# Kernel optimization log

Hardware: AMD Instinct MI355X
Metric: run time of the kernel (lower is better)

## Reference

```python
import jax, jax.numpy as jnp
import numpy as np

B, S, K, N = 4, 2048, 4096, 4096
BLK = 32  # Q4_0 block size along the K (input) dimension


def setup_inputs() -> dict:
    key = jax.random.key(0)
    k1, k2, k3, k4 = jax.random.split(key, 4)
    x = jax.random.normal(k1, (B, S, K), dtype=jnp.float32)
    # 4-bit codes stored unpacked as int32 in [0, 16)
    qweight = jax.random.randint(k2, (N, K), 0, 16, dtype=jnp.int32)
    # one positive fp scale per 32-wide block (typical Q4_0 magnitudes)
    scales = jax.random.uniform(k3, (N, K // BLK), dtype=jnp.float32) * 0.1
    bias = jax.random.normal(k4, (N,), dtype=jnp.float32)
    return {"x": x, "qweight": qweight, "scales": scales, "bias": bias}


def dequantize_q4_0(qweight, scales):
    # w[n, k] = scale[n, k//32] * (q[n, k] - 8)
    n, k = qweight.shape
    q = qweight.reshape(n, k // BLK, BLK).astype(scales.dtype)
    w = (q - 8.0) * scales[:, :, None]
    return w.reshape(n, k)


def reference(x, qweight, scales, bias):
    # dequantize once (cached path), then F.linear(x, w, bias)
    w = dequantize_q4_0(qweight, scales)          # [N, K]
    out = jnp.einsum("bsk,nk->bsn", x, w)          # [B, S, N]
    return out + bias
```

## Files before the change

kernel.cpp:

```cpp
#include <hip/hip_runtime.h>
#include <stdint.h>

#define M_DIM 8192
#define N_DIM 4096
#define K_DIM 4096
#define NKB   (K_DIM / 32)

typedef __bf16 bf16x8 __attribute__((ext_vector_type(8)));
typedef float  f32x4  __attribute__((ext_vector_type(4)));

__device__ __forceinline__ uint32_t pack2_bf16(float lo, float hi) {
    union { float f; uint32_t u; } a, b;
    a.f = lo; b.f = hi;
    return __builtin_amdgcn_perm(b.u + 0x8000u, a.u + 0x8000u, 0x07060302u);
}


__global__ void cvt_x_kernel(const float* __restrict__ x,
                             uint32_t* __restrict__ xb, int n8) {
    int i = blockIdx.x * blockDim.x + threadIdx.x;
    if (i >= n8) return;
    const float4* p = (const float4*)x;
    float4 v0 = p[2 * i], v1 = p[2 * i + 1];
    uint4 o;
    o.x = pack2_bf16(v0.x, v0.y);
    o.y = pack2_bf16(v0.z, v0.w);
    o.z = pack2_bf16(v1.x, v1.y);
    o.w = pack2_bf16(v1.z, v1.w);
    ((uint4*)xb)[i] = o;
}

__global__ void dequant_kernel(const int* __restrict__ q,
                               const float* __restrict__ s,
                               uint32_t* __restrict__ wb, int n8) {
    int i = blockIdx.x * blockDim.x + threadIdx.x;
    if (i >= n8) return;
    int base = i << 3;
    int n = base >> 12;
    int k = base & (K_DIM - 1);
    float sc = s[n * NKB + (k >> 5)];
    float m8 = -8.0f * sc;
    const int4* qp = (const int4*)q;
    int4 q0 = qp[2 * i], q1 = qp[2 * i + 1];
    uint4 o;
    o.x = pack2_bf16(fmaf((float)q0.x, sc, m8), fmaf((float)q0.y, sc, m8));
    o.y = pack2_bf16(fmaf((float)q0.z, sc, m8), fmaf((float)q0.w, sc, m8));
    o.z = pack2_bf16(fmaf((float)q1.x, sc, m8), fmaf((float)q1.y, sc, m8));
    o.w = pack2_bf16(fmaf((float)q1.z, sc, m8), fmaf((float)q1.w, sc, m8));
    ((uint4*)wb)[i] = o;
}

__global__ __launch_bounds__(256)
void gemm_bf16_kernel(const __bf16* __restrict__ A,
                      const __bf16* __restrict__ Bw,
                      const float* __restrict__ bias,
                      float* __restrict__ C) {
    __shared__ __align__(16) __bf16 lA[128 * 32];
    __shared__ __align__(16) __bf16 lB[128 * 32];

    const int t    = threadIdx.x;
    const int wave = t >> 6;
    const int lane = t & 63;
    const int bm = blockIdx.y, bn = blockIdx.x;
    const int wm = wave >> 1, wn = wave & 1;

    const int row0 = t >> 2;
    const int c0   = (t & 3) * 8;
    const __bf16* gA0 = A  + (size_t)(bm * 128 + row0) * K_DIM + c0;
    const __bf16* gA1 = A  + (size_t)(bm * 128 + row0 + 64) * K_DIM + c0;
    const __bf16* gB0 = Bw + (size_t)(bn * 128 + row0) * K_DIM + c0;
    const __bf16* gB1 = Bw + (size_t)(bn * 128 + row0 + 64) * K_DIM + c0;
    __bf16* sA0 = lA + t * 8;
    __bf16* sA1 = lA + (256 + t) * 8;
    __bf16* sB0 = lB + t * 8;
    __bf16* sB1 = lB + (256 + t) * 8;

    const int r = lane & 15, quad = lane >> 4;
    const __bf16* fA = lA + (wm * 64 + r) * 32 + quad * 8;
    const __bf16* fB = lB + (wn * 64 + r) * 32 + quad * 8;

    f32x4 acc[4][4] = {};

    for (int kt = 0; kt < NKB; ++kt) {
        __syncthreads();
        __builtin_amdgcn_global_load_lds(
            (const __attribute__((address_space(1))) uint32_t*)gA0,
            (__attribute__((address_space(3))) uint32_t*)sA0, 16, 0, 0);
        __builtin_amdgcn_global_load_lds(
            (const __attribute__((address_space(1))) uint32_t*)gA1,
            (__attribute__((address_space(3))) uint32_t*)sA1, 16, 0, 0);
        __builtin_amdgcn_global_load_lds(
            (const __attribute__((address_space(1))) uint32_t*)gB0,
            (__attribute__((address_space(3))) uint32_t*)sB0, 16, 0, 0);
        __builtin_amdgcn_global_load_lds(
            (const __attribute__((address_space(1))) uint32_t*)gB1,
            (__attribute__((address_space(3))) uint32_t*)sB1, 16, 0, 0);
        gA0 += 32; gA1 += 32; gB0 += 32; gB1 += 32;
        __syncthreads();

        bf16x8 af[4], bfr[4];
#pragma unroll
        for (int i = 0; i < 4; ++i)
            af[i] = *(const bf16x8*)(fA + i * 16 * 32);
#pragma unroll
        for (int j = 0; j < 4; ++j)
            bfr[j] = *(const bf16x8*)(fB + j * 16 * 32);
#pragma unroll
        for (int i = 0; i < 4; ++i)
#pragma unroll
            for (int j = 0; j < 4; ++j)
                acc[i][j] = __builtin_amdgcn_mfma_f32_16x16x32_bf16(
                    af[i], bfr[j], acc[i][j], 0, 0, 0);
    }

    const int m0 = bm * 128 + wm * 64;
    const int n0 = bn * 128 + wn * 64;
#pragma unroll
    for (int j = 0; j < 4; ++j) {
        int col = n0 + j * 16 + r;
        float bv = bias[col];
#pragma unroll
        for (int i = 0; i < 4; ++i) {
            int rbase = m0 + i * 16 + quad * 4;
#pragma unroll
            for (int e = 0; e < 4; ++e)
                C[(size_t)(rbase + e) * N_DIM + col] = acc[i][j][e] + bv;
        }
    }
}

__global__ __launch_bounds__(256)
void fused_gemm_kernel(const float* __restrict__ X,
                       const int* __restrict__ Q,
                       const float* __restrict__ S,
                       const float* __restrict__ bias,
                       float* __restrict__ C) {
    __shared__ __align__(16) __bf16 lA[128 * 32];
    __shared__ __align__(16) __bf16 lB[128 * 32];

    const int t    = threadIdx.x;
    const int wave = t >> 6;
    const int lane = t & 63;
    const int bm = blockIdx.y, bn = blockIdx.x;
    const int wm = wave >> 1, wn = wave & 1;

    const int srow = t >> 1;
    const int sc0  = (t & 1) << 4;
    const float* gX = X + (size_t)(bm * 128 + srow) * K_DIM + sc0;
    const int*   gQ = Q + (size_t)(bn * 128 + srow) * K_DIM + sc0;
    const float* gS = S + (size_t)(bn * 128 + srow) * NKB;
    __bf16* sA = lA + srow * 32 + sc0;
    __bf16* sB = lB + srow * 32 + sc0;

    const int r = lane & 15, quad = lane >> 4;
    const __bf16* fA = lA + (wm * 64 + r) * 32 + quad * 8;
    const __bf16* fB = lB + (wn * 64 + r) * 32 + quad * 8;

    f32x4 acc[4][4] = {};

    float4 x0 = ((const float4*)gX)[0];
    float4 x1 = ((const float4*)gX)[1];
    float4 x2 = ((const float4*)gX)[2];
    float4 x3 = ((const float4*)gX)[3];
    int4 q0 = ((const int4*)gQ)[0];
    int4 q1 = ((const int4*)gQ)[1];
    int4 q2 = ((const int4*)gQ)[2];
    int4 q3 = ((const int4*)gQ)[3];
    float sc = gS[0];

    for (int kt = 0; kt < NKB; ++kt) {
        uint4 pa0, pa1, pb0, pb1;
        pa0.x = pack2_bf16(x0.x, x0.y); pa0.y = pack2_bf16(x0.z, x0.w);
        pa0.z = pack2_bf16(x1.x, x1.y); pa0.w = pack2_bf16(x1.z, x1.w);
        pa1.x = pack2_bf16(x2.x, x2.y); pa1.y = pack2_bf16(x2.z, x2.w);
        pa1.z = pack2_bf16(x3.x, x3.y); pa1.w = pack2_bf16(x3.z, x3.w);
        float m8 = -8.0f * sc;
        pb0.x = pack2_bf16(fmaf((float)q0.x, sc, m8), fmaf((float)q0.y, sc, m8));
        pb0.y = pack2_bf16(fmaf((float)q0.z, sc, m8), fmaf((float)q0.w, sc, m8));
        pb0.z = pack2_bf16(fmaf((float)q1.x, sc, m8), fmaf((float)q1.y, sc, m8));
        pb0.w = pack2_bf16(fmaf((float)q1.z, sc, m8), fmaf((float)q1.w, sc, m8));
        pb1.x = pack2_bf16(fmaf((float)q2.x, sc, m8), fmaf((float)q2.y, sc, m8));
        pb1.y = pack2_bf16(fmaf((float)q2.z, sc, m8), fmaf((float)q2.w, sc, m8));
        pb1.z = pack2_bf16(fmaf((float)q3.x, sc, m8), fmaf((float)q3.y, sc, m8));
        pb1.w = pack2_bf16(fmaf((float)q3.z, sc, m8), fmaf((float)q3.w, sc, m8));

        __syncthreads();
        *(uint4*)sA = pa0; *(uint4*)(sA + 8) = pa1;
        *(uint4*)sB = pb0; *(uint4*)(sB + 8) = pb1;
        __syncthreads();

        if (kt + 1 < NKB) {
            gX += 32; gQ += 32;
            x0 = ((const float4*)gX)[0];
            x1 = ((const float4*)gX)[1];
            x2 = ((const float4*)gX)[2];
            x3 = ((const float4*)gX)[3];
            q0 = ((const int4*)gQ)[0];
            q1 = ((const int4*)gQ)[1];
            q2 = ((const int4*)gQ)[2];
            q3 = ((const int4*)gQ)[3];
            sc = gS[kt + 1];
        }

        bf16x8 af[4], bfr[4];
#pragma unroll
        for (int i = 0; i < 4; ++i)
            af[i] = *(const bf16x8*)(fA + i * 16 * 32);
#pragma unroll
        for (int j = 0; j < 4; ++j)
            bfr[j] = *(const bf16x8*)(fB + j * 16 * 32);
#pragma unroll
        for (int i = 0; i < 4; ++i)
#pragma unroll
            for (int j = 0; j < 4; ++j)
                acc[i][j] = __builtin_amdgcn_mfma_f32_16x16x32_bf16(
                    af[i], bfr[j], acc[i][j], 0, 0, 0);
    }

    const int m0 = bm * 128 + wm * 64;
    const int n0 = bn * 128 + wn * 64;
#pragma unroll
    for (int j = 0; j < 4; ++j) {
        int col = n0 + j * 16 + r;
        float bv = bias[col];
#pragma unroll
        for (int i = 0; i < 4; ++i) {
            int rbase = m0 + i * 16 + quad * 4;
#pragma unroll
            for (int e = 0; e < 4; ++e)
                C[(size_t)(rbase + e) * N_DIM + col] = acc[i][j][e] + bv;
        }
    }
}

extern "C" void kernel_launch(void* const* d_in, const int* in_sizes, int n_in,
                              void* d_out, int out_size, void* d_ws, size_t ws_size,
                              hipStream_t stream) {
    const float* x    = (const float*)d_in[0];
    const int*   qw   = (const int*)d_in[1];
    const float* sc   = (const float*)d_in[2];
    const float* bias = (const float*)d_in[3];
    float* out = (float*)d_out;

    dim3 grid(N_DIM / 128, M_DIM / 128);

    const size_t need = ((size_t)M_DIM * K_DIM + (size_t)N_DIM * K_DIM) * 2;
    if (ws_size >= need && d_ws != nullptr) {
        uint32_t* xb = (uint32_t*)d_ws;
        uint32_t* wb = xb + (size_t)M_DIM * K_DIM / 2;
        int n8x = M_DIM * K_DIM / 8;
        cvt_x_kernel<<<n8x / 256, 256, 0, stream>>>(x, xb, n8x);
        int n8w = N_DIM * K_DIM / 8;
        dequant_kernel<<<n8w / 256, 256, 0, stream>>>(qw, sc, wb, n8w);
        gemm_bf16_kernel<<<grid, 256, 0, stream>>>(
            (const __bf16*)xb, (const __bf16*)wb, bias, out);
    } else {
        fused_gemm_kernel<<<grid, 256, 0, stream>>>(x, qw, sc, bias, out);
    }
}
```

Measured before the change: 571.0 us.

## Double K tile to 64, XOR-swizzle LDS, overlap next loads with MFMA

The GEMM now stages a 64-wide K slice per iteration instead of 32, halving the number of barrier pairs. LDS is laid out with an XOR swizzle on 16-byte column groups to avoid bank conflicts on fragment reads. Fragments are read into registers first, then the next tile's global-to-LDS loads are issued before the MFMA block so memory latency overlaps compute. The cost is more registers for the doubled fragments, plus a reliance on the async load_lds completing correctly across the barrier.

```diff
diff --git a/kernel.cpp b/kernel.cpp
--- a/kernel.cpp
+++ b/kernel.cpp
@@ -5,6 +5,8 @@
 #define N_DIM 4096
 #define K_DIM 4096
 #define NKB   (K_DIM / 32)
+#define BK    64
+#define KSTEPS (K_DIM / BK)
 
 typedef __bf16 bf16x8 __attribute__((ext_vector_type(8)));
 typedef float  f32x4  __attribute__((ext_vector_type(4)));
@@ -55,8 +57,8 @@
                       const __bf16* __restrict__ Bw,
                       const float* __restrict__ bias,
                       float* __restrict__ C) {
-    __shared__ __align__(16) __bf16 lA[128 * 32];
-    __shared__ __align__(16) __bf16 lB[128 * 32];
+    __shared__ __align__(16) __bf16 lA[128 * BK];
+    __shared__ __align__(16) __bf16 lB[128 * BK];
 
     const int t    = threadIdx.x;
     const int wave = t >> 6;
@@ -64,54 +66,64 @@
     const int bm = blockIdx.y, bn = blockIdx.x;
     const int wm = wave >> 1, wn = wave & 1;
 
-    const int row0 = t >> 2;
-    const int c0   = (t & 3) * 8;
-    const __bf16* gA0 = A  + (size_t)(bm * 128 + row0) * K_DIM + c0;
-    const __bf16* gA1 = A  + (size_t)(bm * 128 + row0 + 64) * K_DIM + c0;
-    const __bf16* gB0 = Bw + (size_t)(bn * 128 + row0) * K_DIM + c0;
-    const __bf16* gB1 = Bw + (size_t)(bn * 128 + row0 + 64) * K_DIM + c0;
-    __bf16* sA0 = lA + t * 8;
-    __bf16* sA1 = lA + (256 + t) * 8;
-    __bf16* sB0 = lB + t * 8;
-    __bf16* sB1 = lB + (256 + t) * 8;
+    const int trow = t >> 3;
+    const int cg   = (t & 7) ^ (trow & 7);
+    const __bf16* gA = A  + (size_t)(bm * 128 + trow) * K_DIM + cg * 8;
+    const __bf16* gB = Bw + (size_t)(bn * 128 + trow) * K_DIM + cg * 8;
+
+#define ISSUE_LOADS()                                                         \
+    do {                                                                      \
+        _Pragma("unroll")                                                     \
+        for (int kk = 0; kk < 4; ++kk) {                                      \
+            __builtin_amdgcn_global_load_lds(                                 \
+                (const __attribute__((address_space(1))) uint32_t*)           \
+                    (gA + (size_t)(32 * kk) * K_DIM),                         \
+                (__attribute__((address_space(3))) uint32_t*)                 \
+                    (lA + (t + 256 * kk) * 8), 16, 0, 0);                     \
+            __builtin_amdgcn_global_load_lds(                                 \
+                (const __attribute__((address_space(1))) uint32_t*)           \
+                    (gB + (size_t)(32 * kk) * K_DIM),                         \
+                (__attribute__((address_space(3))) uint32_t*)                 \
+                    (lB + (t + 256 * kk) * 8), 16, 0, 0);                     \
+        }                                                                     \
+    } while (0)
 
     const int r = lane & 15, quad = lane >> 4;
-    const __bf16* fA = lA + (wm * 64 + r) * 32 + quad * 8;
-    const __bf16* fB = lB + (wn * 64 + r) * 32 + quad * 8;
+    const int s0 = quad ^ (r & 7);
+    const __bf16* fA = lA + (wm * 64 + r) * BK;
+    const __bf16* fB = lB + (wn * 64 + r) * BK;
 
     f32x4 acc[4][4] = {};
 
-    for (int kt = 0; kt < NKB; ++kt) {
-        __syncthreads();
-        __builtin_amdgcn_global_load_lds(
-            (const __attribute__((address_space(1))) uint32_t*)gA0,
-            (__attribute__((address_space(3))) uint32_t*)sA0, 16, 0, 0);
-        __builtin_amdgcn_global_load_lds(
-            (const __attribute__((address_space(1))) uint32_t*)gA1,
-            (__attribute__((address_space(3))) uint32_t*)sA1, 16, 0, 0);
-        __builtin_amdgcn_global_load_lds(
-            (const __attribute__((address_space(1))) uint32_t*)gB0,
-            (__attribute__((address_space(3))) uint32_t*)sB0, 16, 0, 0);
-        __builtin_amdgcn_global_load_lds(
-            (const __attribute__((address_space(1))) uint32_t*)gB1,
-            (__attribute__((address_space(3))) uint32_t*)sB1, 16, 0, 0);
-        gA0 += 32; gA1 += 32; gB0 += 32; gB1 += 32;
-        __syncthreads();
-
-        bf16x8 af[4], bfr[4];
-#pragma unroll
-        for (int i = 0; i < 4; ++i)
-            af[i] = *(const bf16x8*)(fA + i * 16 * 32);
-#pragma unroll
-        for (int j = 0; j < 4; ++j)
-            bfr[j] = *(const bf16x8*)(fB + j * 16 * 32);
-#pragma unroll
-        for (int i = 0; i < 4; ++i)
-#pragma unroll
-            for (int j = 0; j < 4; ++j)
-                acc[i][j] = __builtin_amdgcn_mfma_f32_16x16x32_bf16(
-                    af[i], bfr[j], acc[i][j], 0, 0, 0);
-    }
+    ISSUE_LOADS();
+
+    for (int kt = 0; kt < KSTEPS; ++kt) {
+        __syncthreads();
+        bf16x8 af[2][4], bfr[2][4];
+#pragma unroll
+        for (int i = 0; i < 4; ++i) {
+            af[0][i]  = *(const bf16x8*)(fA + i * 16 * BK + s0 * 8);
+            af[1][i]  = *(const bf16x8*)(fA + i * 16 * BK + (s0 ^ 4) * 8);
+            bfr[0][i] = *(const bf16x8*)(fB + i * 16 * BK + s0 * 8);
+            bfr[1][i] = *(const bf16x8*)(fB + i * 16 * BK + (s0 ^ 4) * 8);
+        }
+        __syncthreads();
+
+        if (kt + 1 < KSTEPS) {
+            gA += BK; gB += BK;
+            ISSUE_LOADS();
+        }
+
+#pragma unroll
+        for (int h = 0; h < 2; ++h)
+#pragma unroll
+            for (int i = 0; i < 4; ++i)
+#pragma unroll
+                for (int j = 0; j < 4; ++j)
+                    acc[i][j] = __builtin_amdgcn_mfma_f32_16x16x32_bf16(
+                        af[h][i], bfr[h][j], acc[i][j], 0, 0, 0);
+    }
+#undef ISSUE_LOADS
 
     const int m0 = bm * 128 + wm * 64;
     const int n0 = bn * 128 + wn * 64;
```

After: 537.1 us. 5.9% less time.
